# Optimization experiments

Measured on AMD Instinct MI355X. Metric: run time of the kernel, lower is better.

The kernel has to match this reference:

```python
import jax, jax.numpy as jnp
import numpy as np

DIM = 1024
D_INNER = 1024
D_STATE = 2048


def setup_inputs() -> dict:
    key = jax.random.key(0)
    ks = jax.random.split(key, 6)
    Bsz, T = 8, 2048
    x = jax.random.normal(ks[0], (Bsz, T, DIM), dtype=jnp.float32)
    h0 = jnp.zeros((Bsz, D_STATE), dtype=jnp.float32)
    # parameters (mamba2_init: normal std=0.02, log_A = 0)
    W_in = jax.random.normal(ks[1], (2 * D_INNER, DIM), dtype=jnp.float32) * 0.02   # nn.Linear weight [out,in]
    W_out = jax.random.normal(ks[2], (DIM, D_INNER), dtype=jnp.float32) * 0.02
    B_mat = jax.random.normal(ks[3], (D_INNER, D_STATE), dtype=jnp.float32) * 0.02
    C_mat = jax.random.normal(ks[4], (D_STATE, D_INNER), dtype=jnp.float32) * 0.02
    log_A = jnp.zeros((D_STATE,), dtype=jnp.float32)
    return {"x": x, "h0": h0, "W_in": W_in, "W_out": W_out,
            "B_mat": B_mat, "C_mat": C_mat, "log_A": log_A}


def reference(x, h0, W_in, W_out, B_mat, C_mat, log_A):
    # x: [B, T, dim]
    xz = jnp.einsum('btd,ed->bte', x, W_in)          # [B, T, 2*d_inner]
    x_proj, z = jnp.split(xz, 2, axis=-1)
    x_proj = jax.nn.silu(x_proj)
    A = jax.nn.sigmoid(log_A)                         # [d_state], fixed (non-selective)

    x_t = jnp.swapaxes(x_proj, 0, 1)                  # [T, B, d_inner]
    z_t = jnp.swapaxes(z, 0, 1)                       # [T, B, d_inner]

    def step(h, xz_t):
        xt, zt = xz_t
        h_new = jnp.tanh(A * h + xt @ B_mat)          # [B, d_state]
        y = (h_new @ C_mat) * jax.nn.silu(zt)         # [B, d_inner]
        return h_new, y

    h_final, y_seq = jax.lax.scan(step, h0, (x_t, z_t))  # y_seq: [T, B, d_inner]
    y = jnp.swapaxes(y_seq, 0, 1)                     # [B, T, d_inner]
    output = jnp.einsum('bti,oi->bto', y, W_out)      # [B, T, dim]
    return output, h_final
```

## Files before the change

kernel.cpp:

```cpp
#include <hip/hip_runtime.h>
#include <cstdint>
#include <cstddef>

#define DIM    1024
#define DINNER 1024
#define DSTATE 2048
#define BSZ    8
#define TLEN   2048
#define MROWS  (BSZ * TLEN)

typedef unsigned short u16;
typedef __attribute__((ext_vector_type(8))) __bf16 bf16x8;
typedef __attribute__((ext_vector_type(4))) float  f32x4;
typedef __attribute__((ext_vector_type(8))) u16    u16x8;

static __device__ __forceinline__ u16 f2bf(float f) {
  union { float f; uint32_t u; } v; v.f = f;
  uint32_t u = v.u;
  return (u16)((u + 0x7fffu + ((u >> 16) & 1u)) >> 16);
}

static __device__ __forceinline__ float bf2f(u16 b) {
  union { uint32_t u; float f; } v; v.u = ((uint32_t)b) << 16;
  return v.f;
}

static __device__ __forceinline__ float silu(float x) {
  return x / (1.f + __expf(-x));
}

__global__ void sentinel(float* out) { out[0] = 12345.0f; }


__global__ void cast_bf16x8(const float* __restrict__ in, u16* __restrict__ out, long n) {
  long i = ((long)blockIdx.x * blockDim.x + threadIdx.x) * 8;
  if (i >= n) return;
  float4 a = *(const float4*)(in + i);
  float4 b = *(const float4*)(in + i + 4);
  u16x8 o;
  o[0] = f2bf(a.x); o[1] = f2bf(a.y); o[2] = f2bf(a.z); o[3] = f2bf(a.w);
  o[4] = f2bf(b.x); o[5] = f2bf(b.y); o[6] = f2bf(b.z); o[7] = f2bf(b.w);
  *(u16x8*)(out + i) = o;
}

__global__ void transpose_cast(const float* __restrict__ in, u16* __restrict__ out,
                               int R, int C) {
  __shared__ float t[32][33];
  int c0 = blockIdx.x * 32, r0 = blockIdx.y * 32;
  int tx = threadIdx.x, ty = threadIdx.y;
#pragma unroll
  for (int i = 0; i < 32; i += 8)
    t[ty + i][tx] = in[(size_t)(r0 + ty + i) * C + c0 + tx];
  __syncthreads();
#pragma unroll
  for (int i = 0; i < 32; i += 8)
    out[(size_t)(c0 + ty + i) * R + r0 + tx] = f2bf(t[tx][ty + i]);
}


#define SEG  128
#define WARM 32

__global__ void __launch_bounds__(256) winscan(const u16* __restrict__ xB,
                                               u16* __restrict__ H,
                                               const float* __restrict__ h0,
                                               const float* __restrict__ logA,
                                               float* __restrict__ hf,
                                               int b0) {
  const int NSEG = TLEN / SEG;
  int tid  = blockIdx.x * 256 + threadIdx.x;
  int s    = tid & (DSTATE - 1);
  int rest = tid >> 11;
  int bl   = rest >> 4;
  int seg  = rest & (NSEG - 1);

  const float C2  = 2.8853900817779268f;
  const float L2E = 1.4426950408889634f;
  float A  = __builtin_amdgcn_rcpf(1.f + __builtin_amdgcn_exp2f(-logA[s] * L2E));
  float Ac = A * C2;

  const int t0 = seg * SEG;
  float h;
  const u16* src;
  if (seg == 0) {
    h = h0[(size_t)(b0 + bl) * DSTATE + s];
    src = xB + ((size_t)bl * TLEN) * DSTATE + s;
  } else {
    h = 0.f;
    src = xB + ((size_t)bl * TLEN + (t0 - WARM)) * DSTATE + s;
#pragma unroll
    for (int i = 0; i < WARM; ++i) {
      float g = fmaf(Ac, h, bf2f(src[(size_t)i * DSTATE]) * C2);
      float e = __builtin_amdgcn_exp2f(g);
      float r = __builtin_amdgcn_rcpf(e + 1.f);
      h = fmaf(-2.f, r, 1.f);
    }
    src += (size_t)WARM * DSTATE;
  }

  u16* dst = H + ((size_t)bl * TLEN + t0) * DSTATE + s;
  const int PF = 8;
  float buf[PF], nbuf[PF];
#pragma unroll
  for (int i = 0; i < PF; ++i) buf[i] = bf2f(src[(size_t)i * DSTATE]) * C2;
  for (int tc = 0; tc < SEG; tc += PF) {
    if (tc + PF < SEG) {
#pragma unroll
      for (int i = 0; i < PF; ++i) nbuf[i] = bf2f(src[(size_t)(tc + PF + i) * DSTATE]) * C2;
    }
#pragma unroll
    for (int i = 0; i < PF; ++i) {
      float g = fmaf(Ac, h, buf[i]);
      float e = __builtin_amdgcn_exp2f(g);
      float r = __builtin_amdgcn_rcpf(e + 1.f);
      h = fmaf(-2.f, r, 1.f);
      dst[(size_t)(tc + i) * DSTATE] = f2bf(h);
    }
#pragma unroll
    for (int i = 0; i < PF; ++i) buf[i] = nbuf[i];
  }
  if (seg == NSEG - 1) hf[(size_t)(b0 + bl) * DSTATE + s] = h;
}


enum { EPI_F32 = 0, EPI_SILU_SPLIT = 1, EPI_BF16 = 2, EPI_MUL_SZ = 3 };

#define GBARS() do { __builtin_amdgcn_s_barrier(); \
                     __builtin_amdgcn_sched_barrier(0); } while (0)

template <int EPI>
__global__ void __launch_bounds__(512, 2) gemm256(const u16* __restrict__ A,
                                                  const u16* __restrict__ B,
                                                  float* __restrict__ Cf,
                                                  u16* __restrict__ O1,
                                                  u16* __restrict__ O2,
                                                  const u16* __restrict__ SZ,
                                                  int M, int N, int K) {
  extern __shared__ u16 lds[];
  const int tid = threadIdx.x, wid = tid >> 6, lane = tid & 63;
  const int wm = wid >> 2, wn = wid & 3;

  int bx = blockIdx.x, by = blockIdx.y;
  {
    int gx = gridDim.x, gy = gridDim.y;
    int nwg = gx * gy;
    int wg  = blockIdx.y * gx + blockIdx.x;
    if ((nwg & 7) == 0) {
      int v = (wg & 7) * (nwg >> 3) + (wg >> 3);
      bx = v / gy;
      by = v - bx * gy;
    }
  }
  const int m0 = bx * 256, n0 = by * 256;

  const int fr = lane & 15;
  const int kbs8 = ((lane >> 4) ^ ((fr >> 1) & 3)) * 8;
  const int srow = tid >> 2, skb = tid & 3;

  f32x4 acc[8][4] = {};
  bf16x8 af[8], bfj[4];

  auto STG = [&](int db, int mat, int ks, int kt) {
#pragma unroll
    for (int c = 0; c < 2; ++c) {
      int row = c * 128 + srow;
      int ksrc8 = (skb ^ ((row >> 1) & 3)) * 8;
      const u16* P = mat ? B : A;
      const u16* g = P + (size_t)((mat ? n0 : m0) + row) * K + (kt << 6) + (ks << 5) + ksrc8;
      u16* d = lds + (((db * 2 + mat) * 2 + ks) << 13) + (c << 12) + (wid << 9);
      __builtin_amdgcn_global_load_lds((const __attribute__((address_space(1))) void*)g,
          (__attribute__((address_space(3))) void*)d, 16, 0, 0);
    }
  };
  auto LDA = [&](int db, int ks) {
    const u16* base = lds + (((db * 2 + 0) * 2 + ks) << 13) + (wm * 128 + fr) * 32 + kbs8;
#pragma unroll
    for (int i = 0; i < 8; ++i) af[i] = *(const bf16x8*)(base + i * 512);
  };
  auto LDB4 = [&](int db, int ks) {
    const u16* base = lds + (((db * 2 + 1) * 2 + ks) << 13) + (wn * 64 + fr) * 32 + kbs8;
#pragma unroll
    for (int j = 0; j < 4; ++j) bfj[j] = *(const bf16x8*)(base + j * 512);
  };
  auto MM = [&](int jp) {
    __builtin_amdgcn_s_setprio(1);
#pragma unroll
    for (int i = 0; i < 8; ++i) {
      acc[i][jp * 2]     = __builtin_amdgcn_mfma_f32_16x16x32_bf16(af[i], bfj[jp * 2],     acc[i][jp * 2],     0, 0, 0);
      acc[i][jp * 2 + 1] = __builtin_amdgcn_mfma_f32_16x16x32_bf16(af[i], bfj[jp * 2 + 1], acc[i][jp * 2 + 1], 0, 0, 0);
    }
    __builtin_amdgcn_s_setprio(0);
  };

  const int T = K >> 6;
  const int I = T >> 1;

  STG(0, 0, 0, 0); STG(0, 1, 0, 0); STG(0, 0, 1, 0); STG(0, 1, 1, 0);
  STG(1, 0, 0, 1); STG(1, 1, 0, 1); STG(1, 0, 1, 1);
  asm volatile("s_waitcnt vmcnt(6)" ::: "memory");

  for (int it = 0; it < I; ++it) {
    const bool last = (it == I - 1);
    const int t1 = 2 * it + 1, t2 = 2 * it + 2, t3 = 2 * it + 3;

    GBARS(); STG(1, 1, 1, t1); LDA(0, 0); LDB4(0, 0); MM(0);
    GBARS(); if (!last) STG(0, 0, 0, t2); MM(1);

    GBARS(); if (!last) STG(0, 1, 0, t2); LDA(0, 1); LDB4(0, 1); MM(0);
    GBARS(); if (!last) STG(0, 0, 1, t2);
    if (last) { asm volatile("s_waitcnt vmcnt(0)" ::: "memory"); }
    else      { asm volatile("s_waitcnt vmcnt(6)" ::: "memory"); }
    MM(1);

    GBARS(); if (!last) STG(0, 1, 1, t2); LDA(1, 0); LDB4(1, 0); MM(0);
    GBARS(); if (!last) STG(1, 0, 0, t3); MM(1);

    GBARS(); if (!last) STG(1, 1, 0, t3); LDA(1, 1); LDB4(1, 1); MM(0);
    GBARS();
    if (!last) { STG(1, 0, 1, t3); asm volatile("s_waitcnt vmcnt(6)" ::: "memory"); }
    MM(1);
  }
  GBARS();

  {
    float* esl = (float*)lds + wid * (16 * 66);
    const int cr = (lane >> 4) * 4;
    const int cc = lane & 15;
    const int erow = lane >> 2;
    const int ecol = (lane & 3) * 16;
#pragma unroll
    for (int i = 0; i < 8; ++i) {
#pragma unroll
      for (int j = 0; j < 4; ++j)
#pragma unroll
        for (int r = 0; r < 4; ++r)
          esl[(cr + r) * 66 + j * 16 + cc] = acc[i][j][r];
      asm volatile("s_waitcnt lgkmcnt(0)" ::: "memory");
      __builtin_amdgcn_sched_barrier(0);
      f32x4 v0 = *(const f32x4*)(esl + erow * 66 + ecol);
      f32x4 v1 = *(const f32x4*)(esl + erow * 66 + ecol + 4);
      f32x4 v2 = *(const f32x4*)(esl + erow * 66 + ecol + 8);
      f32x4 v3 = *(const f32x4*)(esl + erow * 66 + ecol + 12);
      asm volatile("s_waitcnt lgkmcnt(0)" ::: "memory");
      __builtin_amdgcn_sched_barrier(0);
      const int gm = m0 + wm * 128 + i * 16 + erow;
      const int gn = n0 + wn * 64 + ecol;
      if constexpr (EPI == EPI_F32) {
        float* cp = Cf + (size_t)gm * N + gn;
        *(f32x4*)(cp)      = v0;
        *(f32x4*)(cp + 4)  = v1;
        *(f32x4*)(cp + 8)  = v2;
        *(f32x4*)(cp + 12) = v3;
      } else if constexpr (EPI == EPI_BF16) {
        u16x8 o1, o2;
#pragma unroll
        for (int r = 0; r < 4; ++r) { o1[r] = f2bf(v0[r]); o1[4 + r] = f2bf(v1[r]); }
#pragma unroll
        for (int r = 0; r < 4; ++r) { o2[r] = f2bf(v2[r]); o2[4 + r] = f2bf(v3[r]); }
        u16* op = O1 + (size_t)gm * N + gn;
        *(u16x8*)(op) = o1;
        *(u16x8*)(op + 8) = o2;
      } else if constexpr (EPI == EPI_SILU_SPLIT) {
        u16x8 o1, o2;
#pragma unroll
        for (int r = 0; r < 4; ++r) { o1[r] = f2bf(silu(v0[r])); o1[4 + r] = f2bf(silu(v1[r])); }
#pragma unroll
        for (int r = 0; r < 4; ++r) { o2[r] = f2bf(silu(v2[r])); o2[4 + r] = f2bf(silu(v3[r])); }
        const int half = N >> 1;
        u16* op = (gn < half ? O1 + (size_t)gm * half + gn
                             : O2 + (size_t)gm * half + (gn - half));
        *(u16x8*)(op) = o1;
        *(u16x8*)(op + 8) = o2;
      } else {
        const u16* sp = SZ + (size_t)gm * N + gn;
        u16x8 s1 = *(const u16x8*)(sp);
        u16x8 s2 = *(const u16x8*)(sp + 8);
        u16x8 o1, o2;
#pragma unroll
        for (int r = 0; r < 4; ++r) { o1[r] = f2bf(v0[r] * bf2f(s1[r])); o1[4 + r] = f2bf(v1[r] * bf2f(s1[4 + r])); }
#pragma unroll
        for (int r = 0; r < 4; ++r) { o2[r] = f2bf(v2[r] * bf2f(s2[r])); o2[4 + r] = f2bf(v3[r] * bf2f(s2[4 + r])); }
        u16* op = O1 + (size_t)gm * N + gn;
        *(u16x8*)(op) = o1;
        *(u16x8*)(op + 8) = o2;
      }
    }
  }
}


extern "C" void kernel_launch(void* const* d_in, const int* in_sizes, int n_in,
                              void* d_out, int out_size, void* d_ws, size_t ws_size,
                              hipStream_t stream) {
  const float* x     = (const float*)d_in[0];
  const float* h0    = (const float*)d_in[1];
  const float* W_in  = (const float*)d_in[2];
  const float* W_out = (const float*)d_in[3];
  const float* Bm    = (const float*)d_in[4];
  const float* Cm    = (const float*)d_in[5];
  const float* logA  = (const float*)d_in[6];
  float* out = (float*)d_out;
  float* hf  = out + (size_t)MROWS * DIM;

  const int LDSB = 131072;
  hipFuncSetAttribute((const void*)gemm256<EPI_F32>,        hipFuncAttributeMaxDynamicSharedMemorySize, LDSB);
  hipFuncSetAttribute((const void*)gemm256<EPI_SILU_SPLIT>, hipFuncAttributeMaxDynamicSharedMemorySize, LDSB);
  hipFuncSetAttribute((const void*)gemm256<EPI_BF16>,       hipFuncAttributeMaxDynamicSharedMemorySize, LDSB);
  hipFuncSetAttribute((const void*)gemm256<EPI_MUL_SZ>,     hipFuncAttributeMaxDynamicSharedMemorySize, LDSB);

  auto align256 = [](size_t b) { return (b + 255) & ~(size_t)255; };

  const size_t w_win  = align256((size_t)2 * DINNER * DIM * 2);
  const size_t w_wout = align256((size_t)DIM * DINNER * 2);
  const size_t w_bt   = align256((size_t)DSTATE * DINNER * 2);
  const size_t w_ct   = align256((size_t)DINNER * DSTATE * 2);
  const size_t w_weights = w_win + w_wout + w_bt + w_ct;

  int nb = 0;
  const int cand[4] = {8, 4, 2, 1};
  size_t su = 0, sx = 0, ssz = 0, sxb = 0;
  for (int ci = 0; ci < 4; ++ci) {
    int c = cand[ci];
    size_t Mc = (size_t)c * TLEN;
    su  = (size_t)Mc * DINNER * 2;
    sx  = (size_t)Mc * DINNER * 2;
    ssz = (size_t)Mc * DINNER * 2;
    sxb = (size_t)Mc * DSTATE * 2;
    if (w_weights + su + sx + ssz + sxb <= ws_size) { nb = c; break; }
  }
  if (!nb) { sentinel<<<1, 1, 0, stream>>>(out); return; }

  char* ws = (char*)d_ws;
  u16* Win_bf  = (u16*)ws;             ws += w_win;
  u16* Wout_bf = (u16*)ws;             ws += w_wout;
  u16* BT_bf   = (u16*)ws;             ws += w_bt;
  u16* CT_bf   = (u16*)ws;             ws += w_ct;
  u16* u_bf    = (u16*)ws;             ws += su;
  u16* x_bf    = (u16*)ws;             ws += sx;
  u16* sz_bf   = (u16*)ws;             ws += ssz;
  u16* xB_bf   = (u16*)ws;             ws += sxb;
  u16* H_bf    = u_bf;
  u16* y_bf    = xB_bf;

  cast_bf16x8<<<(2 * DINNER * DIM) / 8 / 256, 256, 0, stream>>>(W_in, Win_bf, (long)2 * DINNER * DIM);
  cast_bf16x8<<<(DIM * DINNER) / 8 / 256, 256, 0, stream>>>(W_out, Wout_bf, (long)DIM * DINNER);
  transpose_cast<<<dim3(DSTATE / 32, DINNER / 32), dim3(32, 8), 0, stream>>>(Bm, BT_bf, DINNER, DSTATE);
  transpose_cast<<<dim3(DINNER / 32, DSTATE / 32), dim3(32, 8), 0, stream>>>(Cm, CT_bf, DSTATE, DINNER);

  for (int b0 = 0; b0 < BSZ; b0 += nb) {
    const int Mc = nb * TLEN;
    const float* xc = x + (size_t)b0 * TLEN * DIM;
    float* outc = out + (size_t)b0 * TLEN * DIM;

    cast_bf16x8<<<((size_t)Mc * DIM) / 8 / 256, 256, 0, stream>>>(xc, x_bf, (long)Mc * DIM);

    gemm256<EPI_SILU_SPLIT><<<dim3(Mc / 256, (2 * DINNER) / 256), 512, LDSB, stream>>>(
        x_bf, Win_bf, nullptr, u_bf, sz_bf, nullptr, Mc, 2 * DINNER, DIM);

    gemm256<EPI_BF16><<<dim3(Mc / 256, DSTATE / 256), 512, LDSB, stream>>>(
        u_bf, BT_bf, nullptr, xB_bf, nullptr, nullptr, Mc, DSTATE, DINNER);

    winscan<<<Mc / 16, 256, 0, stream>>>(xB_bf, H_bf, h0, logA, hf, b0);

    gemm256<EPI_MUL_SZ><<<dim3(Mc / 256, DINNER / 256), 512, LDSB, stream>>>(
        H_bf, CT_bf, nullptr, y_bf, nullptr, sz_bf, Mc, DINNER, DSTATE);

    gemm256<EPI_F32><<<dim3(Mc / 256, DIM / 256), 512, LDSB, stream>>>(
        y_bf, Wout_bf, outc, nullptr, nullptr, nullptr, Mc, DIM, DINNER);
  }
}
```

Baseline: 342.2 us.

## Double-buffer LDS-to-register fragments to overlap ds_reads with MFMA

Adds a second set of register fragments for A and B so the next k-substep's LDS reads are issued while the current substep's MFMAs run. The prologue preloads the first fragments, and the global-load wait counts and barrier placement are reshuffled to match the new staging order. This is meant to hide LDS read latency behind matrix math in the GEMM. In exchange it uses more VGPRs, which can lower occupancy or cause spills, and the revised vmcnt and barrier schedule must still cover every LDS buffer reuse.

```diff
diff --git a/kernel.cpp b/kernel.cpp
--- a/kernel.cpp
+++ b/kernel.cpp
@@ -158,7 +158,7 @@
   const int srow = tid >> 2, skb = tid & 3;
 
   f32x4 acc[8][4] = {};
-  bf16x8 af[8], bfj[4];
+  bf16x8 afA[8], afB[8], bfA[4], bfB[4];
 
   auto STG = [&](int db, int mat, int ks, int kt) {
 #pragma unroll
@@ -172,22 +172,22 @@
           (__attribute__((address_space(3))) void*)d, 16, 0, 0);
     }
   };
-  auto LDA = [&](int db, int ks) {
+  auto LDRA = [&](bf16x8* dst, int db, int ks) {
     const u16* base = lds + (((db * 2 + 0) * 2 + ks) << 13) + (wm * 128 + fr) * 32 + kbs8;
 #pragma unroll
-    for (int i = 0; i < 8; ++i) af[i] = *(const bf16x8*)(base + i * 512);
+    for (int i = 0; i < 8; ++i) dst[i] = *(const bf16x8*)(base + i * 512);
   };
-  auto LDB4 = [&](int db, int ks) {
+  auto LDRB = [&](bf16x8* dst, int db, int ks) {
     const u16* base = lds + (((db * 2 + 1) * 2 + ks) << 13) + (wn * 64 + fr) * 32 + kbs8;
 #pragma unroll
-    for (int j = 0; j < 4; ++j) bfj[j] = *(const bf16x8*)(base + j * 512);
+    for (int j = 0; j < 4; ++j) dst[j] = *(const bf16x8*)(base + j * 512);
   };
-  auto MM = [&](int jp) {
+  auto MMh = [&](const bf16x8* afb, const bf16x8* bfb, int jp) {
     __builtin_amdgcn_s_setprio(1);
 #pragma unroll
     for (int i = 0; i < 8; ++i) {
-      acc[i][jp * 2]     = __builtin_amdgcn_mfma_f32_16x16x32_bf16(af[i], bfj[jp * 2],     acc[i][jp * 2],     0, 0, 0);
-      acc[i][jp * 2 + 1] = __builtin_amdgcn_mfma_f32_16x16x32_bf16(af[i], bfj[jp * 2 + 1], acc[i][jp * 2 + 1], 0, 0, 0);
+      acc[i][jp * 2]     = __builtin_amdgcn_mfma_f32_16x16x32_bf16(afb[i], bfb[jp * 2],     acc[i][jp * 2],     0, 0, 0);
+      acc[i][jp * 2 + 1] = __builtin_amdgcn_mfma_f32_16x16x32_bf16(afb[i], bfb[jp * 2 + 1], acc[i][jp * 2 + 1], 0, 0, 0);
     }
     __builtin_amdgcn_s_setprio(0);
   };
@@ -198,27 +198,26 @@
   STG(0, 0, 0, 0); STG(0, 1, 0, 0); STG(0, 0, 1, 0); STG(0, 1, 1, 0);
   STG(1, 0, 0, 1); STG(1, 1, 0, 1); STG(1, 0, 1, 1);
   asm volatile("s_waitcnt vmcnt(6)" ::: "memory");
+  GBARS();
+  LDRA(afA, 0, 0); LDRB(bfA, 0, 0);
 
   for (int it = 0; it < I; ++it) {
     const bool last = (it == I - 1);
     const int t1 = 2 * it + 1, t2 = 2 * it + 2, t3 = 2 * it + 3;
 
-    GBARS(); STG(1, 1, 1, t1); LDA(0, 0); LDB4(0, 0); MM(0);
-    GBARS(); if (!last) STG(0, 0, 0, t2); MM(1);
-
-    GBARS(); if (!last) STG(0, 1, 0, t2); LDA(0, 1); LDB4(0, 1); MM(0);
-    GBARS(); if (!last) STG(0, 0, 1, t2);
+    GBARS(); STG(1, 1, 1, t1); MMh(afA, bfA, 0);
+    GBARS(); if (!last) STG(0, 0, 0, t2); LDRA(afB, 0, 1); LDRB(bfB, 0, 1); MMh(afA, bfA, 1);
+    GBARS(); if (!last) STG(0, 1, 0, t2); MMh(afB, bfB, 0);
     if (last) { asm volatile("s_waitcnt vmcnt(0)" ::: "memory"); }
-    else      { asm volatile("s_waitcnt vmcnt(6)" ::: "memory"); }
-    MM(1);
-
-    GBARS(); if (!last) STG(0, 1, 1, t2); LDA(1, 0); LDB4(1, 0); MM(0);
-    GBARS(); if (!last) STG(1, 0, 0, t3); MM(1);
-
-    GBARS(); if (!last) STG(1, 1, 0, t3); LDA(1, 1); LDB4(1, 1); MM(0);
+    else      { asm volatile("s_waitcnt vmcnt(4)" ::: "memory"); }
+    GBARS(); if (!last) STG(0, 0, 1, t2); LDRA(afA, 1, 0); LDRB(bfA, 1, 0); MMh(afB, bfB, 1);
+    GBARS(); if (!last) STG(0, 1, 1, t2); MMh(afA, bfA, 0);
+    GBARS(); if (!last) STG(1, 0, 0, t3); LDRA(afB, 1, 1); LDRB(bfB, 1, 1); MMh(afA, bfA, 1);
+    GBARS(); if (!last) STG(1, 1, 0, t3); MMh(afB, bfB, 0);
+    if (!last) { asm volatile("s_waitcnt vmcnt(4)" ::: "memory"); }
     GBARS();
-    if (!last) { STG(1, 0, 1, t3); asm volatile("s_waitcnt vmcnt(6)" ::: "memory"); }
-    MM(1);
+    if (!last) { STG(1, 0, 1, t3); LDRA(afA, 0, 0); LDRB(bfA, 0, 0); }
+    MMh(afB, bfB, 1);
   }
   GBARS();
 
```

Result: slower. 386.6 us (+13.0%).

## Switch GEMM inner loop from 16x16x32 to 32x32x16 bf16 MFMA

Applied to the files above, without the earlier changes.

Replaces the 16x16x32 MFMA tiling with 32x32x16 MFMA instructions. The per-wave LDS fragment loads change to 32-row fragments split into two K halves, and the epilogue is remapped to the 32x32 accumulator layout. The larger MFMA shape needs fewer LDS reads per FLOP and has higher per-instruction throughput on CDNA. The cost is a more complex accumulator-to-row mapping in the epilogue and different LDS bank access patterns under the existing swizzle.

```diff
diff --git a/kernel.cpp b/kernel.cpp
--- a/kernel.cpp
+++ b/kernel.cpp
@@ -10,9 +10,10 @@
 #define MROWS  (BSZ * TLEN)
 
 typedef unsigned short u16;
-typedef __attribute__((ext_vector_type(8))) __bf16 bf16x8;
-typedef __attribute__((ext_vector_type(4))) float  f32x4;
-typedef __attribute__((ext_vector_type(8))) u16    u16x8;
+typedef __attribute__((ext_vector_type(8)))  __bf16 bf16x8;
+typedef __attribute__((ext_vector_type(4)))  float  f32x4;
+typedef __attribute__((ext_vector_type(16))) float  f32x16;
+typedef __attribute__((ext_vector_type(8)))  u16    u16x8;
 
 static __device__ __forceinline__ u16 f2bf(float f) {
   union { float f; uint32_t u; } v; v.f = f;
@@ -153,12 +154,12 @@
   }
   const int m0 = bx * 256, n0 = by * 256;
 
-  const int fr = lane & 15;
-  const int kbs8 = ((lane >> 4) ^ ((fr >> 1) & 3)) * 8;
+  const int ln31 = lane & 31;
+  const int kg   = lane >> 5;
   const int srow = tid >> 2, skb = tid & 3;
 
-  f32x4 acc[8][4] = {};
-  bf16x8 af[8], bfj[4];
+  f32x16 acc[4][2] = {};
+  bf16x8 af0[4], af1[4], bf0[2], bf1[2];
 
   auto STG = [&](int db, int mat, int ks, int kt) {
 #pragma unroll
@@ -172,23 +173,44 @@
           (__attribute__((address_space(3))) void*)d, 16, 0, 0);
     }
   };
-  auto LDA = [&](int db, int ks) {
-    const u16* base = lds + (((db * 2 + 0) * 2 + ks) << 13) + (wm * 128 + fr) * 32 + kbs8;
-#pragma unroll
-    for (int i = 0; i < 8; ++i) af[i] = *(const bf16x8*)(base + i * 512);
-  };
-  auto LDB4 = [&](int db, int ks) {
-    const u16* base = lds + (((db * 2 + 1) * 2 + ks) << 13) + (wn * 64 + fr) * 32 + kbs8;
-#pragma unroll
-    for (int j = 0; j < 4; ++j) bfj[j] = *(const bf16x8*)(base + j * 512);
-  };
-  auto MM = [&](int jp) {
+  auto LDA2 = [&](int db, int ks) {
+    const u16* base = lds + (((db * 2 + 0) * 2 + ks) << 13);
+#pragma unroll
+    for (int i = 0; i < 4; ++i) {
+      int row = wm * 128 + i * 32 + ln31;
+      int sw = (row >> 1) & 3;
+      const u16* rb = base + row * 32;
+      af0[i] = *(const bf16x8*)(rb + ((kg) ^ sw) * 8);
+      af1[i] = *(const bf16x8*)(rb + ((2 + kg) ^ sw) * 8);
+    }
+  };
+  auto LDB2 = [&](int db, int ks) {
+    const u16* base = lds + (((db * 2 + 1) * 2 + ks) << 13);
+#pragma unroll
+    for (int j = 0; j < 2; ++j) {
+      int row = wn * 64 + j * 32 + ln31;
+      int sw = (row >> 1) & 3;
+      const u16* rb = base + row * 32;
+      bf0[j] = *(const bf16x8*)(rb + ((kg) ^ sw) * 8);
+      bf1[j] = *(const bf16x8*)(rb + ((2 + kg) ^ sw) * 8);
+    }
+  };
+  auto MM0 = [&]() {
     __builtin_amdgcn_s_setprio(1);
 #pragma unroll
-    for (int i = 0; i < 8; ++i) {
-      acc[i][jp * 2]     = __builtin_amdgcn_mfma_f32_16x16x32_bf16(af[i], bfj[jp * 2],     acc[i][jp * 2],     0, 0, 0);
-      acc[i][jp * 2 + 1] = __builtin_amdgcn_mfma_f32_16x16x32_bf16(af[i], bfj[jp * 2 + 1], acc[i][jp * 2 + 1], 0, 0, 0);
-    }
+    for (int i = 0; i < 4; ++i)
+#pragma unroll
+      for (int j = 0; j < 2; ++j)
+        acc[i][j] = __builtin_amdgcn_mfma_f32_32x32x16_bf16(af0[i], bf0[j], acc[i][j], 0, 0, 0);
+    __builtin_amdgcn_s_setprio(0);
+  };
+  auto MM1 = [&]() {
+    __builtin_amdgcn_s_setprio(1);
+#pragma unroll
+    for (int i = 0; i < 4; ++i)
+#pragma unroll
+      for (int j = 0; j < 2; ++j)
+        acc[i][j] = __builtin_amdgcn_mfma_f32_32x32x16_bf16(af1[i], bf1[j], acc[i][j], 0, 0, 0);
     __builtin_amdgcn_s_setprio(0);
   };
 
@@ -203,88 +225,90 @@
     const bool last = (it == I - 1);
     const int t1 = 2 * it + 1, t2 = 2 * it + 2, t3 = 2 * it + 3;
 
-    GBARS(); STG(1, 1, 1, t1); LDA(0, 0); LDB4(0, 0); MM(0);
-    GBARS(); if (!last) STG(0, 0, 0, t2); MM(1);
-
-    GBARS(); if (!last) STG(0, 1, 0, t2); LDA(0, 1); LDB4(0, 1); MM(0);
+    GBARS(); STG(1, 1, 1, t1); LDA2(0, 0); LDB2(0, 0); MM0();
+    GBARS(); if (!last) STG(0, 0, 0, t2); MM1();
+
+    GBARS(); if (!last) STG(0, 1, 0, t2); LDA2(0, 1); LDB2(0, 1); MM0();
     GBARS(); if (!last) STG(0, 0, 1, t2);
     if (last) { asm volatile("s_waitcnt vmcnt(0)" ::: "memory"); }
     else      { asm volatile("s_waitcnt vmcnt(6)" ::: "memory"); }
-    MM(1);
-
-    GBARS(); if (!last) STG(0, 1, 1, t2); LDA(1, 0); LDB4(1, 0); MM(0);
-    GBARS(); if (!last) STG(1, 0, 0, t3); MM(1);
-
-    GBARS(); if (!last) STG(1, 1, 0, t3); LDA(1, 1); LDB4(1, 1); MM(0);
+    MM1();
+
+    GBARS(); if (!last) STG(0, 1, 1, t2); LDA2(1, 0); LDB2(1, 0); MM0();
+    GBARS(); if (!last) STG(1, 0, 0, t3); MM1();
+
+    GBARS(); if (!last) STG(1, 1, 0, t3); LDA2(1, 1); LDB2(1, 1); MM0();
     GBARS();
     if (!last) { STG(1, 0, 1, t3); asm volatile("s_waitcnt vmcnt(6)" ::: "memory"); }
-    MM(1);
+    MM1();
   }
   GBARS();
 
   {
     float* esl = (float*)lds + wid * (16 * 66);
-    const int cr = (lane >> 4) * 4;
-    const int cc = lane & 15;
     const int erow = lane >> 2;
     const int ecol = (lane & 3) * 16;
 #pragma unroll
-    for (int i = 0; i < 8; ++i) {
-#pragma unroll
-      for (int j = 0; j < 4; ++j)
-#pragma unroll
-        for (int r = 0; r < 4; ++r)
-          esl[(cr + r) * 66 + j * 16 + cc] = acc[i][j][r];
-      asm volatile("s_waitcnt lgkmcnt(0)" ::: "memory");
-      __builtin_amdgcn_sched_barrier(0);
-      f32x4 v0 = *(const f32x4*)(esl + erow * 66 + ecol);
-      f32x4 v1 = *(const f32x4*)(esl + erow * 66 + ecol + 4);
-      f32x4 v2 = *(const f32x4*)(esl + erow * 66 + ecol + 8);
-      f32x4 v3 = *(const f32x4*)(esl + erow * 66 + ecol + 12);
-      asm volatile("s_waitcnt lgkmcnt(0)" ::: "memory");
-      __builtin_amdgcn_sched_barrier(0);
-      const int gm = m0 + wm * 128 + i * 16 + erow;
-      const int gn = n0 + wn * 64 + ecol;
-      if constexpr (EPI == EPI_F32) {
-        float* cp = Cf + (size_t)gm * N + gn;
-        *(f32x4*)(cp)      = v0;
-        *(f32x4*)(cp + 4)  = v1;
-        *(f32x4*)(cp + 8)  = v2;
-        *(f32x4*)(cp + 12) = v3;
-      } else if constexpr (EPI == EPI_BF16) {
-        u16x8 o1, o2;
-#pragma unroll
-        for (int r = 0; r < 4; ++r) { o1[r] = f2bf(v0[r]); o1[4 + r] = f2bf(v1[r]); }
-#pragma unroll
-        for (int r = 0; r < 4; ++r) { o2[r] = f2bf(v2[r]); o2[4 + r] = f2bf(v3[r]); }
-        u16* op = O1 + (size_t)gm * N + gn;
-        *(u16x8*)(op) = o1;
-        *(u16x8*)(op + 8) = o2;
-      } else if constexpr (EPI == EPI_SILU_SPLIT) {
-        u16x8 o1, o2;
-#pragma unroll
-        for (int r = 0; r < 4; ++r) { o1[r] = f2bf(silu(v0[r])); o1[4 + r] = f2bf(silu(v1[r])); }
-#pragma unroll
-        for (int r = 0; r < 4; ++r) { o2[r] = f2bf(silu(v2[r])); o2[4 + r] = f2bf(silu(v3[r])); }
-        const int half = N >> 1;
-        u16* op = (gn < half ? O1 + (size_t)gm * half + gn
-                             : O2 + (size_t)gm * half + (gn - half));
-        *(u16x8*)(op) = o1;
-        *(u16x8*)(op + 8) = o2;
-      } else {
-        const u16* sp = SZ + (size_t)gm * N + gn;
-        u16x8 s1 = *(const u16x8*)(sp);
-        u16x8 s2 = *(const u16x8*)(sp + 8);
-        u16x8 o1, o2;
-#pragma unroll
-        for (int r = 0; r < 4; ++r) { o1[r] = f2bf(v0[r] * bf2f(s1[r])); o1[4 + r] = f2bf(v1[r] * bf2f(s1[4 + r])); }
-#pragma unroll
-        for (int r = 0; r < 4; ++r) { o2[r] = f2bf(v2[r] * bf2f(s2[r])); o2[4 + r] = f2bf(v3[r] * bf2f(s2[4 + r])); }
-        u16* op = O1 + (size_t)gm * N + gn;
-        *(u16x8*)(op) = o1;
-        *(u16x8*)(op + 8) = o2;
+    for (int i4 = 0; i4 < 4; ++i4)
+#pragma unroll
+      for (int h = 0; h < 2; ++h) {
+#pragma unroll
+        for (int j = 0; j < 2; ++j)
+#pragma unroll
+          for (int q = 0; q < 8; ++q) {
+            int r16 = (q & 3) + 8 * (q >> 2) + 4 * (lane >> 5);
+            esl[r16 * 66 + j * 32 + ln31] = acc[i4][j][h * 8 + q];
+          }
+        asm volatile("s_waitcnt lgkmcnt(0)" ::: "memory");
+        __builtin_amdgcn_sched_barrier(0);
+        f32x4 v0 = *(const f32x4*)(esl + erow * 66 + ecol);
+        f32x4 v1 = *(const f32x4*)(esl + erow * 66 + ecol + 4);
+        f32x4 v2 = *(const f32x4*)(esl + erow * 66 + ecol + 8);
+        f32x4 v3 = *(const f32x4*)(esl + erow * 66 + ecol + 12);
+        asm volatile("s_waitcnt lgkmcnt(0)" ::: "memory");
+        __builtin_amdgcn_sched_barrier(0);
+        const int gm = m0 + wm * 128 + i4 * 32 + h * 16 + erow;
+        const int gn = n0 + wn * 64 + ecol;
+        if constexpr (EPI == EPI_F32) {
+          float* cp = Cf + (size_t)gm * N + gn;
+          *(f32x4*)(cp)      = v0;
+          *(f32x4*)(cp + 4)  = v1;
+          *(f32x4*)(cp + 8)  = v2;
+          *(f32x4*)(cp + 12) = v3;
+        } else if constexpr (EPI == EPI_BF16) {
+          u16x8 o1, o2;
+#pragma unroll
+          for (int r = 0; r < 4; ++r) { o1[r] = f2bf(v0[r]); o1[4 + r] = f2bf(v1[r]); }
+#pragma unroll
+          for (int r = 0; r < 4; ++r) { o2[r] = f2bf(v2[r]); o2[4 + r] = f2bf(v3[r]); }
+          u16* op = O1 + (size_t)gm * N + gn;
+          *(u16x8*)(op) = o1;
+          *(u16x8*)(op + 8) = o2;
+        } else if constexpr (EPI == EPI_SILU_SPLIT) {
+          u16x8 o1, o2;
+#pragma unroll
+          for (int r = 0; r < 4; ++r) { o1[r] = f2bf(silu(v0[r])); o1[4 + r] = f2bf(silu(v1[r])); }
+#pragma unroll
+          for (int r = 0; r < 4; ++r) { o2[r] = f2bf(silu(v2[r])); o2[4 + r] = f2bf(silu(v3[r])); }
+          const int half = N >> 1;
+          u16* op = (gn < half ? O1 + (size_t)gm * half + gn
+                               : O2 + (size_t)gm * half + (gn - half));
+          *(u16x8*)(op) = o1;
+          *(u16x8*)(op + 8) = o2;
+        } else {
+          const u16* sp = SZ + (size_t)gm * N + gn;
+          u16x8 s1 = *(const u16x8*)(sp);
+          u16x8 s2 = *(const u16x8*)(sp + 8);
+          u16x8 o1, o2;
+#pragma unroll
+          for (int r = 0; r < 4; ++r) { o1[r] = f2bf(v0[r] * bf2f(s1[r])); o1[4 + r] = f2bf(v1[r] * bf2f(s1[4 + r])); }
+#pragma unroll
+          for (int r = 0; r < 4; ++r) { o2[r] = f2bf(v2[r] * bf2f(s2[r])); o2[4 + r] = f2bf(v3[r] * bf2f(s2[4 + r])); }
+          u16* op = O1 + (size_t)gm * N + gn;
+          *(u16x8*)(op) = o1;
+          *(u16x8*)(op + 8) = o2;
+        }
       }
-    }
   }
 }
 
```

Result: slower. 369.5 us (+8.0%).
